# Performance work log

Measured on AMD Instinct MI355X. Metric: run time of the kernel, lower is better.

Reference implementation:

```python
import jax, jax.numpy as jnp
from jax import lax
import numpy as np

B, T, K = 512, 512, 64


def setup_inputs() -> dict:
    key = jax.random.key(0)
    k1, k2, k3, k4 = jax.random.split(key, 4)
    return {
        "emissions": jax.random.normal(k1, (B, T, K), dtype=jnp.float32),
        "attn_mask": jnp.ones((B, T), dtype=jnp.int32),
        "start_transitions": jax.random.normal(k2, (K,), dtype=jnp.float32) * 0.1,
        "end_transitions": jax.random.normal(k3, (K,), dtype=jnp.float32) * 0.1,
        "transitions": jax.random.normal(k4, (K, K), dtype=jnp.float32) * 0.1,
    }


def reference(emissions, attn_mask, start_transitions, end_transitions, transitions):
    """Viterbi decode (torchcrf CRF.decode). Returns best tag paths [B, T] int32."""
    mask = attn_mask.astype(bool)  # [B, T]; mask[:, 0] assumed all True (torchcrf requirement)
    score0 = start_transitions[None, :] + emissions[:, 0]  # [B, K]

    emits = jnp.swapaxes(emissions[:, 1:], 0, 1)  # [T-1, B, K]
    masks = jnp.swapaxes(mask[:, 1:], 0, 1)       # [T-1, B]

    def viterbi_step(score, xs):
        emit_t, mask_t = xs                                        # [B,K], [B]
        cand = score[:, :, None] + transitions[None, :, :] + emit_t[:, None, :]  # [B,Kprev,Knext]
        next_score = cand.max(axis=1)                              # [B, K]
        idx = cand.argmax(axis=1).astype(jnp.int32)                # [B, K] best prev tag
        new_score = jnp.where(mask_t[:, None], next_score, score)  # freeze past seq end
        return new_score, idx

    final_score, history = lax.scan(viterbi_step, score0, (emits, masks))
    final_score = final_score + end_transitions[None, :]           # [B, K]
    best_last = jnp.argmax(final_score, axis=1).astype(jnp.int32)  # [B]

    def backtrace_step(tag, xs):
        idx_t, mask_t = xs  # [B, K], [B]
        prev = jnp.take_along_axis(idx_t, tag[:, None], axis=1)[:, 0]
        new_tag = jnp.where(mask_t, prev, tag)
        return new_tag, new_tag

    _, tags_prefix = lax.scan(backtrace_step, best_last, (history, masks), reverse=True)
    tags = jnp.concatenate([tags_prefix, best_last[None, :]], axis=0)  # [T, B]
    return jnp.swapaxes(tags, 0, 1)  # [B, T]
```

## Files before the change

kernel.cpp:

```cpp
#include <hip/hip_runtime.h>
#include <hip/hip_bf16.h>


#define TT 512
#define BB 512
#define KK 64
#define RS 68

#define NEG_INF (-3.402823466e38f)

__global__ __launch_bounds__(64) void viterbi_fwd(
    const float* __restrict__ emissions,
    const int* __restrict__ attn_mask,
    const float* __restrict__ start_t,
    const float* __restrict__ end_t,
    const float* __restrict__ trans,
    unsigned char* __restrict__ hist,
    int* __restrict__ best_last)
{
    const int b = blockIdx.x;
    const int j = threadIdx.x & 63;

    __shared__ __align__(16) float ldsT[KK * RS];
    __shared__ float sv[KK];

#pragma unroll 4
    for (int i = 0; i < KK; ++i)
        ldsT[j * RS + i] = trans[i * KK + j];
    __syncthreads();

    const float* row = &ldsT[j * RS];

    const float* eb = emissions + (size_t)b * TT * KK;
    const int*   mb = attn_mask + (size_t)b * TT;
    unsigned char* hb = hist + (size_t)b * TT * KK;

    float score = start_t[j] + eb[j];

    float e0 = eb[KK + j];
    float e1 = eb[2 * KK + j];
    int   m0 = mb[1];
    int   m1 = mb[2];

    for (int t = 1; t < TT; ++t) {
        float e = e0; e0 = e1;
        int   m = m0; m0 = m1;
        int tn = (t + 2 < TT) ? (t + 2) : (TT - 1);
        e1 = eb[(size_t)tn * KK + j];
        m1 = mb[tn];

        unsigned off = 0;
        asm volatile("" : "+v"(off));
        const float* rb = row + off;

#define LDQ(q) (*(const float4*)(rb + 4 * (q)))
#define BC(i)  __uint_as_float(__builtin_amdgcn_ds_bpermute(4 * (i), __float_as_uint(score)))

        float gv[8];
        int   gi[8];

        float4 qa0 = LDQ(0), qa1 = LDQ(1), qb0 = LDQ(2), qb1 = LDQ(3);
#pragma unroll
        for (int g = 0; g < 8; ++g) {
            float4 p0 = qa0, p1 = qa1;
            if (g < 6) { p0 = LDQ(2 * g + 4); p1 = LDQ(2 * g + 5); }

            const int base = 8 * g;
            float bv = (BC(base + 0) + qa0.x) + e; int bi = base;
            float c;
            c = (BC(base + 1) + qa0.y) + e; if (c > bv) { bv = c; bi = base + 1; }
            c = (BC(base + 2) + qa0.z) + e; if (c > bv) { bv = c; bi = base + 2; }
            c = (BC(base + 3) + qa0.w) + e; if (c > bv) { bv = c; bi = base + 3; }
            c = (BC(base + 4) + qa1.x) + e; if (c > bv) { bv = c; bi = base + 4; }
            c = (BC(base + 5) + qa1.y) + e; if (c > bv) { bv = c; bi = base + 5; }
            c = (BC(base + 6) + qa1.z) + e; if (c > bv) { bv = c; bi = base + 6; }
            c = (BC(base + 7) + qa1.w) + e; if (c > bv) { bv = c; bi = base + 7; }
            gv[g] = bv;
            gi[g] = bi;

            qa0 = qb0; qa1 = qb1; qb0 = p0; qb1 = p1;
        }

        float best = gv[0];
        int   bi   = gi[0];
#pragma unroll
        for (int g = 1; g < 8; ++g)
            if (gv[g] > best) { best = gv[g]; bi = gi[g]; }

#undef LDQ
#undef BC

        hb[(size_t)(t - 1) * KK + j] = (unsigned char)bi;
        score = m ? best : score;
    }

    float fin = score + end_t[j];
    sv[j] = fin;
    __syncthreads();
    if (j == 0) {
        float bv = sv[0];
        int   bt = 0;
#pragma unroll
        for (int k = 1; k < KK; ++k) {
            float v = sv[k];
            if (v > bv) { bv = v; bt = k; }
        }
        best_last[b] = bt;
    }
}

__global__ __launch_bounds__(64) void viterbi_bt(
    const unsigned char* __restrict__ hist,
    const int* __restrict__ attn_mask,
    const int* __restrict__ best_last,
    int* __restrict__ out)
{
    const int b = blockIdx.x;
    const int l = threadIdx.x;
    __shared__ int path[TT];

    const unsigned int* hw = (const unsigned int*)(hist + (size_t)b * TT * KK);
    const int* mb = attn_mask + (size_t)b * TT;

    int tag = best_last[b];
    if (l == 0) path[TT - 1] = tag;

    unsigned int dwA[16], dwB[16];
    int mA, mB;

    auto loadChunk = [&](int c, unsigned int (&dw)[16], int& mreg) {
#pragma unroll
        for (int q4 = 0; q4 < 16; ++q4)
            dw[q4] = hw[c * 1024 + q4 * 64 + l];
        int midx = c * 64 + l + 1;
        if (midx > TT - 1) midx = TT - 1;
        mreg = mb[midx];
    };
    auto procChunk = [&](int c, unsigned int (&dw)[16], int mreg) {
#pragma unroll
        for (int q = 63; q >= 0; --q) {
            int r = c * 64 + q;
            if (r < TT - 1) {
                unsigned int d = __shfl(dw[q >> 2], ((q & 3) << 4) + (tag >> 2));
                int pv = (int)((d >> ((tag & 3) << 3)) & 0xFFu);
                int m  = __shfl(mreg, q);
                tag = m ? pv : tag;
                if (l == 0) path[r] = tag;
            }
        }
    };

    loadChunk(7, dwA, mA);
    for (int c = 7; c >= 1; c -= 2) {
        loadChunk(c - 1, dwB, mB);
        procChunk(c, dwA, mA);
        if (c >= 2) loadChunk(c - 2, dwA, mA);
        procChunk(c - 1, dwB, mB);
    }

    __syncthreads();
#pragma unroll
    for (int cc = 0; cc < 8; ++cc)
        out[(size_t)b * TT + cc * 64 + l] = path[cc * 64 + l];
}

extern "C" void kernel_launch(void* const* d_in, const int* in_sizes, int n_in,
                              void* d_out, int out_size, void* d_ws, size_t ws_size,
                              hipStream_t stream) {
    const float* emissions = (const float*)d_in[0];
    const int* attn_mask   = (const int*)d_in[1];
    const float* start_t   = (const float*)d_in[2];
    const float* end_t     = (const float*)d_in[3];
    const float* trans     = (const float*)d_in[4];
    int* out = (int*)d_out;

    unsigned char* hist = (unsigned char*)d_ws;
    int* best_last = (int*)((char*)d_ws + (size_t)BB * TT * KK);

    viterbi_fwd<<<BB, KK, 0, stream>>>(emissions, attn_mask, start_t, end_t,
                                       trans, hist, best_last);
    viterbi_bt<<<BB, KK, 0, stream>>>(hist, attn_mask, best_last, out);
}
```

Baseline: 504.6 us.

## Process two batch sequences per wavefront in Viterbi forward pass

Each forward block now handles two batch rows at once, interleaving their max/argmax chains so the transition rows loaded from LDS are shared and the two independent dependency chains hide each other's bpermute latency. The grid is halved to 256 blocks, which on a 256-CU device gives one wave per CU. This trades parallelism (fewer waves to hide latency across) for per-wave ILP and more register pressure.

Result: slower. 856.3 us (+69.7%).

```diff
diff --git a/kernel.cpp b/kernel.cpp
--- a/kernel.cpp
+++ b/kernel.cpp
@@ -9,7 +9,7 @@
 
 #define NEG_INF (-3.402823466e38f)
 
-__global__ __launch_bounds__(64) void viterbi_fwd(
+__global__ __launch_bounds__(64, 1) void viterbi_fwd(
     const float* __restrict__ emissions,
     const int* __restrict__ attn_mask,
     const float* __restrict__ start_t,
@@ -18,7 +18,8 @@
     unsigned char* __restrict__ hist,
     int* __restrict__ best_last)
 {
-    const int b = blockIdx.x;
+    const int bp = blockIdx.x;
+    const int bA = 2 * bp, bB = 2 * bp + 1;
     const int j = threadIdx.x & 63;
 
     __shared__ __align__(16) float ldsT[KK * RS];
@@ -31,33 +32,42 @@
 
     const float* row = &ldsT[j * RS];
 
-    const float* eb = emissions + (size_t)b * TT * KK;
-    const int*   mb = attn_mask + (size_t)b * TT;
-    unsigned char* hb = hist + (size_t)b * TT * KK;
-
-    float score = start_t[j] + eb[j];
-
-    float e0 = eb[KK + j];
-    float e1 = eb[2 * KK + j];
-    int   m0 = mb[1];
-    int   m1 = mb[2];
+    const float* ebA = emissions + (size_t)bA * TT * KK;
+    const float* ebB = emissions + (size_t)bB * TT * KK;
+    const int*   mbA = attn_mask + (size_t)bA * TT;
+    const int*   mbB = attn_mask + (size_t)bB * TT;
+    unsigned char* hbA = hist + (size_t)bA * TT * KK;
+    unsigned char* hbB = hist + (size_t)bB * TT * KK;
+
+    float sA = start_t[j] + ebA[j];
+    float sB = start_t[j] + ebB[j];
+
+    float e0A = ebA[KK + j], e1A = ebA[2 * KK + j];
+    float e0B = ebB[KK + j], e1B = ebB[2 * KK + j];
+    int   m0A = mbA[1], m1A = mbA[2];
+    int   m0B = mbB[1], m1B = mbB[2];
 
     for (int t = 1; t < TT; ++t) {
-        float e = e0; e0 = e1;
-        int   m = m0; m0 = m1;
+        float eA = e0A; e0A = e1A;
+        float eB = e0B; e0B = e1B;
+        int   mA_ = m0A; m0A = m1A;
+        int   mB_ = m0B; m0B = m1B;
         int tn = (t + 2 < TT) ? (t + 2) : (TT - 1);
-        e1 = eb[(size_t)tn * KK + j];
-        m1 = mb[tn];
+        e1A = ebA[(size_t)tn * KK + j];
+        e1B = ebB[(size_t)tn * KK + j];
+        m1A = mbA[tn];
+        m1B = mbB[tn];
 
         unsigned off = 0;
         asm volatile("" : "+v"(off));
         const float* rb = row + off;
 
 #define LDQ(q) (*(const float4*)(rb + 4 * (q)))
-#define BC(i)  __uint_as_float(__builtin_amdgcn_ds_bpermute(4 * (i), __float_as_uint(score)))
-
-        float gv[8];
-        int   gi[8];
+#define BCA(i) __uint_as_float(__builtin_amdgcn_ds_bpermute(4 * (i), __float_as_uint(sA)))
+#define BCB(i) __uint_as_float(__builtin_amdgcn_ds_bpermute(4 * (i), __float_as_uint(sB)))
+
+        float gvA[8]; int giA[8];
+        float gvB[8]; int giB[8];
 
         float4 qa0 = LDQ(0), qa1 = LDQ(1), qb0 = LDQ(2), qb1 = LDQ(3);
 #pragma unroll
@@ -66,46 +76,71 @@
             if (g < 6) { p0 = LDQ(2 * g + 4); p1 = LDQ(2 * g + 5); }
 
             const int base = 8 * g;
-            float bv = (BC(base + 0) + qa0.x) + e; int bi = base;
             float c;
-            c = (BC(base + 1) + qa0.y) + e; if (c > bv) { bv = c; bi = base + 1; }
-            c = (BC(base + 2) + qa0.z) + e; if (c > bv) { bv = c; bi = base + 2; }
-            c = (BC(base + 3) + qa0.w) + e; if (c > bv) { bv = c; bi = base + 3; }
-            c = (BC(base + 4) + qa1.x) + e; if (c > bv) { bv = c; bi = base + 4; }
-            c = (BC(base + 5) + qa1.y) + e; if (c > bv) { bv = c; bi = base + 5; }
-            c = (BC(base + 6) + qa1.z) + e; if (c > bv) { bv = c; bi = base + 6; }
-            c = (BC(base + 7) + qa1.w) + e; if (c > bv) { bv = c; bi = base + 7; }
-            gv[g] = bv;
-            gi[g] = bi;
+            float bvA = (BCA(base + 0) + qa0.x) + eA; int iA = base;
+            float bvB = (BCB(base + 0) + qa0.x) + eB; int iB = base;
+            c = (BCA(base + 1) + qa0.y) + eA; if (c > bvA) { bvA = c; iA = base + 1; }
+            c = (BCB(base + 1) + qa0.y) + eB; if (c > bvB) { bvB = c; iB = base + 1; }
+            c = (BCA(base + 2) + qa0.z) + eA; if (c > bvA) { bvA = c; iA = base + 2; }
+            c = (BCB(base + 2) + qa0.z) + eB; if (c > bvB) { bvB = c; iB = base + 2; }
+            c = (BCA(base + 3) + qa0.w) + eA; if (c > bvA) { bvA = c; iA = base + 3; }
+            c = (BCB(base + 3) + qa0.w) + eB; if (c > bvB) { bvB = c; iB = base + 3; }
+            c = (BCA(base + 4) + qa1.x) + eA; if (c > bvA) { bvA = c; iA = base + 4; }
+            c = (BCB(base + 4) + qa1.x) + eB; if (c > bvB) { bvB = c; iB = base + 4; }
+            c = (BCA(base + 5) + qa1.y) + eA; if (c > bvA) { bvA = c; iA = base + 5; }
+            c = (BCB(base + 5) + qa1.y) + eB; if (c > bvB) { bvB = c; iB = base + 5; }
+            c = (BCA(base + 6) + qa1.z) + eA; if (c > bvA) { bvA = c; iA = base + 6; }
+            c = (BCB(base + 6) + qa1.z) + eB; if (c > bvB) { bvB = c; iB = base + 6; }
+            c = (BCA(base + 7) + qa1.w) + eA; if (c > bvA) { bvA = c; iA = base + 7; }
+            c = (BCB(base + 7) + qa1.w) + eB; if (c > bvB) { bvB = c; iB = base + 7; }
+            gvA[g] = bvA; giA[g] = iA;
+            gvB[g] = bvB; giB[g] = iB;
 
             qa0 = qb0; qa1 = qb1; qb0 = p0; qb1 = p1;
         }
 
-        float best = gv[0];
-        int   bi   = gi[0];
-#pragma unroll
-        for (int g = 1; g < 8; ++g)
-            if (gv[g] > best) { best = gv[g]; bi = gi[g]; }
+        float bestA = gvA[0]; int wiA = giA[0];
+        float bestB = gvB[0]; int wiB = giB[0];
+#pragma unroll
+        for (int g = 1; g < 8; ++g) {
+            if (gvA[g] > bestA) { bestA = gvA[g]; wiA = giA[g]; }
+            if (gvB[g] > bestB) { bestB = gvB[g]; wiB = giB[g]; }
+        }
 
 #undef LDQ
-#undef BC
-
-        hb[(size_t)(t - 1) * KK + j] = (unsigned char)bi;
-        score = m ? best : score;
-    }
-
-    float fin = score + end_t[j];
-    sv[j] = fin;
+#undef BCA
+#undef BCB
+
+        hbA[(size_t)(t - 1) * KK + j] = (unsigned char)wiA;
+        hbB[(size_t)(t - 1) * KK + j] = (unsigned char)wiB;
+        sA = mA_ ? bestA : sA;
+        sB = mB_ ? bestB : sB;
+    }
+
+    float finA = sA + end_t[j];
+    sv[j] = finA;
     __syncthreads();
     if (j == 0) {
-        float bv = sv[0];
-        int   bt = 0;
+        float bv = sv[0]; int bt = 0;
 #pragma unroll
         for (int k = 1; k < KK; ++k) {
             float v = sv[k];
             if (v > bv) { bv = v; bt = k; }
         }
-        best_last[b] = bt;
+        best_last[bA] = bt;
+    }
+    __syncthreads();
+    float finB = sB + end_t[j];
+    sv[j] = finB;
+    __syncthreads();
+    if (j == 0) {
+        float bv = sv[0]; int bt = 0;
+#pragma unroll
+        for (int k = 1; k < KK; ++k) {
+            float v = sv[k];
+            if (v > bv) { bv = v; bt = k; }
+        }
+        best_last[bB] = bt;
     }
 }
 
@@ -177,7 +212,7 @@
     unsigned char* hist = (unsigned char*)d_ws;
     int* best_last = (int*)((char*)d_ws + (size_t)BB * TT * KK);
 
-    viterbi_fwd<<<BB, KK, 0, stream>>>(emissions, attn_mask, start_t, end_t,
-                                       trans, hist, best_last);
+    viterbi_fwd<<<BB / 2, KK, 0, stream>>>(emissions, attn_mask, start_t, end_t,
+                                           trans, hist, best_last);
     viterbi_bt<<<BB, KK, 0, stream>>>(hist, attn_mask, best_last, out);
 }
```
